# Kernel tuning notes

Hardware: AMD Instinct MI355X
Metric: run time of the kernel (lower is better)

Reference implementation:

```python
import jax, jax.numpy as jnp
import numpy as np

N_NODES = 50000
N_EDGES = 800000
D = 128
N_STEPS = 3
N_ETYPES = 4


def setup_inputs() -> dict:
    key = jax.random.key(0)
    ks = jax.random.split(key, 8)
    feat = jax.random.normal(ks[0], (N_NODES, D), dtype=jnp.float32)
    # per-edge-type linear weights, xavier-ish scale
    W_lin = jax.random.normal(ks[1], (N_ETYPES, D, D), dtype=jnp.float32) * (1.0 / np.sqrt(D))
    b_lin = jnp.zeros((N_ETYPES, D), dtype=jnp.float32)
    # GRUCell params (torch layout: [3*D, D] rows ordered r, z, n)
    s = 1.0 / np.sqrt(D)
    w_ih = jax.random.uniform(ks[2], (3 * D, D), dtype=jnp.float32, minval=-s, maxval=s)
    w_hh = jax.random.uniform(ks[3], (3 * D, D), dtype=jnp.float32, minval=-s, maxval=s)
    b_ih = jax.random.uniform(ks[4], (3 * D,), dtype=jnp.float32, minval=-s, maxval=s)
    b_hh = jax.random.uniform(ks[5], (3 * D,), dtype=jnp.float32, minval=-s, maxval=s)
    src = jax.random.randint(ks[6], (N_EDGES,), 0, N_NODES, dtype=jnp.int32)
    dst = jax.random.randint(ks[7], (N_EDGES,), 0, N_NODES, dtype=jnp.int32)
    etypes = jax.random.randint(jax.random.fold_in(key, 99), (N_EDGES,), 0, N_ETYPES, dtype=jnp.int32)
    return {"feat": feat, "W_lin": W_lin, "b_lin": b_lin, "w_ih": w_ih,
            "w_hh": w_hh, "b_ih": b_ih, "b_hh": b_hh,
            "src": src, "dst": dst, "etypes": etypes}


def _gru_cell(a, h, w_ih, w_hh, b_ih, b_hh):
    # torch.nn.GRUCell math; gates ordered r, z, n
    gi = a @ w_ih.T + b_ih   # [N, 3D]
    gh = h @ w_hh.T + b_hh   # [N, 3D]
    ir, iz, inn = jnp.split(gi, 3, axis=-1)
    hr, hz, hn = jnp.split(gh, 3, axis=-1)
    r = jax.nn.sigmoid(ir + hr)
    z = jax.nn.sigmoid(iz + hz)
    n = jnp.tanh(inn + r * hn)
    return (1.0 - z) * n + z * h


def reference(feat, W_lin, b_lin, w_ih, w_hh, b_ih, b_hh, src, dst, etypes):
    n_nodes = feat.shape[0]
    h = feat  # in_feats == out_feats, so zero_pad is empty
    for _ in range(N_STEPS):
        hs = h[src]  # gather source node features [E, D]
        # per-edge-type linear: W_etype @ h_src + b_etype
        m = jnp.zeros_like(hs)
        for i in range(N_ETYPES):
            mi = hs @ W_lin[i].T + b_lin[i]
            m = jnp.where((etypes == i)[:, None], mi, m)
        # sparse sum aggregation onto destination nodes
        a = jax.ops.segment_sum(m, dst, num_segments=n_nodes)
        h = _gru_cell(a, h, w_ih, w_hh, b_ih, b_hh)
    return h
```

## Files before the change

kernel.cpp:

```cpp
#include <hip/hip_runtime.h>
#include <hip/hip_bf16.h>
#include <math.h>
#include <stdint.h>

#define NNODES 50000
#define NEDGES 800000
#define DIM 128
#define NB_SCAN 98

typedef __attribute__((ext_vector_type(8))) short bf16x8;
typedef __attribute__((ext_vector_type(4))) float f32x4;

__device__ __forceinline__ short f2bf(float f) {
    unsigned int u = __float_as_uint(f);
    u += 0x7FFFu + ((u >> 16) & 1u);
    return (short)(u >> 16);
}

__global__ __launch_bounds__(256)
void conv_swz_w(const float* __restrict__ W, unsigned short* __restrict__ out,
                int nunits) {
    const int u = blockIdx.x * 256 + threadIdx.x;
    if (u >= nunits) return;
    const int cb = u >> 11;
    const int ul = u & 2047;
    const int fi = ul >> 8;
    const int ks = (ul >> 6) & 3;
    const int ln = ul & 63;
    const int row = cb * 128 + fi * 16 + (ln & 15);
    const int col = ks * 32 + (ln >> 4) * 8;
    const float4 f0 = *(const float4*)(W + (size_t)row * DIM + col);
    const float4 f1 = *(const float4*)(W + (size_t)row * DIM + col + 4);
    bf16x8 v;
    v[0] = f2bf(f0.x); v[1] = f2bf(f0.y); v[2] = f2bf(f0.z); v[3] = f2bf(f0.w);
    v[4] = f2bf(f1.x); v[5] = f2bf(f1.y); v[6] = f2bf(f1.z); v[7] = f2bf(f1.w);
    *(bf16x8*)(out + (size_t)u * 8) = v;
}

template<typename InT, typename OutT>
__global__ __launch_bounds__(256, 2)
void gemm_mfma_bias(const InT* __restrict__ A, const unsigned short* __restrict__ Bswz,
                    const float* __restrict__ bias, OutT* __restrict__ C,
                    int M, int N) {
    __shared__ short lsA[128 * 128];
    __shared__ short lsB[128 * 128];
    const int t = threadIdx.x;
    const int bm = blockIdx.x * 128;
    const int bn = blockIdx.y * 128;

    const unsigned short* Bblk = Bswz + (size_t)blockIdx.y * (2048 * 8);
    #pragma unroll
    for (int i = 0; i < 8; ++i) {
        const int u = i * 256 + t;
        *(bf16x8*)(lsB + (size_t)u * 8) = *(const bf16x8*)(Bblk + (size_t)u * 8);
    }
    #pragma unroll
    for (int i = 0; i < 8; ++i) {
        const int u = i * 256 + t;
        const int fi = u >> 8;
        const int ks = (u >> 6) & 3;
        const int ln = u & 63;
        const int r = ln & 15;
        const int gk = ks * 32 + (ln >> 4) * 8;
        const int grow = bm + fi * 16 + r;
        bf16x8 va = {0, 0, 0, 0, 0, 0, 0, 0};
        if (grow < M) {
            if constexpr (sizeof(InT) == 2) {
                va = *(const bf16x8*)(A + (size_t)grow * DIM + gk);
            } else {
                const float4 f0 = *(const float4*)(A + (size_t)grow * DIM + gk);
                const float4 f1 = *(const float4*)(A + (size_t)grow * DIM + gk + 4);
                va[0] = f2bf(f0.x); va[1] = f2bf(f0.y); va[2] = f2bf(f0.z); va[3] = f2bf(f0.w);
                va[4] = f2bf(f1.x); va[5] = f2bf(f1.y); va[6] = f2bf(f1.z); va[7] = f2bf(f1.w);
            }
        }
        *(bf16x8*)(lsA + (size_t)u * 8) = va;
    }
    __syncthreads();

    const int lane = t & 63;
    const int wave = t >> 6;
    const int wm = wave >> 1;
    const int wn = wave & 1;

    f32x4 acc[4][4];
    #pragma unroll
    for (int mi = 0; mi < 4; ++mi)
        #pragma unroll
        for (int nj = 0; nj < 4; ++nj)
            acc[mi][nj] = (f32x4){0.f, 0.f, 0.f, 0.f};

    #pragma unroll
    for (int ks = 0; ks < 4; ++ks) {
        bf16x8 af[4], bfr[4];
        #pragma unroll
        for (int mi = 0; mi < 4; ++mi)
            af[mi] = *(const bf16x8*)(lsA + (size_t)((((wm * 4 + mi) * 4 + ks) * 64 + lane)) * 8);
        #pragma unroll
        for (int nj = 0; nj < 4; ++nj)
            bfr[nj] = *(const bf16x8*)(lsB + (size_t)((((wn * 4 + nj) * 4 + ks) * 64 + lane)) * 8);
        #pragma unroll
        for (int mi = 0; mi < 4; ++mi)
            #pragma unroll
            for (int nj = 0; nj < 4; ++nj)
                acc[mi][nj] = __builtin_amdgcn_mfma_f32_16x16x32_bf16(
                    af[mi], bfr[nj], acc[mi][nj], 0, 0, 0);
    }

    const int cr = lane >> 4;
    const int cc = lane & 15;
    float bv[4];
    #pragma unroll
    for (int nj = 0; nj < 4; ++nj)
        bv[nj] = bias[bn + wn * 64 + nj * 16 + cc];

    #pragma unroll
    for (int mi = 0; mi < 4; ++mi) {
        const int row0 = bm + wm * 64 + mi * 16 + cr * 4;
        #pragma unroll
        for (int reg = 0; reg < 4; ++reg) {
            const int row = row0 + reg;
            if (row >= M) continue;
            #pragma unroll
            for (int nj = 0; nj < 4; ++nj) {
                const int col = bn + wn * 64 + nj * 16 + cc;
                const float v = acc[mi][nj][reg] + bv[nj];
                if constexpr (sizeof(OutT) == 2)
                    C[(size_t)row * N + col] = (OutT)f2bf(v);
                else
                    C[(size_t)row * N + col] = v;
            }
        }
    }
}

__global__ __launch_bounds__(256)
void hist_dst(const int* __restrict__ dst, int* __restrict__ cnt) {
    const int e = blockIdx.x * 256 + threadIdx.x;
    if (e < NEDGES) atomicAdd(&cnt[dst[e]], 1);
}

__global__ __launch_bounds__(256)
void scan_blksum(const int* __restrict__ cnt, int* __restrict__ partial) {
    __shared__ int red[256];
    const int b = blockIdx.x, t = threadIdx.x;
    const int i0 = b * 512 + t * 2;
    const int v0 = (i0 < NNODES) ? cnt[i0] : 0;
    const int v1 = (i0 + 1 < NNODES) ? cnt[i0 + 1] : 0;
    red[t] = v0 + v1;
    __syncthreads();
    for (int off = 128; off > 0; off >>= 1) {
        if (t < off) red[t] += red[t + off];
        __syncthreads();
    }
    if (t == 0) partial[b] = red[0];
}

__global__ __launch_bounds__(128)
void scan_partials(const int* __restrict__ partial, int* __restrict__ bloff) {
    __shared__ int s[128];
    const int t = threadIdx.x;
    s[t] = (t < NB_SCAN) ? partial[t] : 0;
    __syncthreads();
    for (int off = 1; off < 128; off <<= 1) {
        const int v = (t >= off) ? s[t - off] : 0;
        __syncthreads();
        s[t] += v;
        __syncthreads();
    }
    if (t < NB_SCAN) bloff[t] = (t == 0) ? 0 : s[t - 1];
}

__global__ __launch_bounds__(256)
void scan_final(const int* __restrict__ cnt, const int* __restrict__ bloff,
                int* __restrict__ row_start, int* __restrict__ cursor) {
    __shared__ int s[256];
    const int b = blockIdx.x, t = threadIdx.x;
    const int i0 = b * 512 + t * 2;
    const int v0 = (i0 < NNODES) ? cnt[i0] : 0;
    const int v1 = (i0 + 1 < NNODES) ? cnt[i0 + 1] : 0;
    s[t] = v0 + v1;
    __syncthreads();
    for (int off = 1; off < 256; off <<= 1) {
        const int v = (t >= off) ? s[t - off] : 0;
        __syncthreads();
        s[t] += v;
        __syncthreads();
    }
    const int excl = bloff[b] + ((t == 0) ? 0 : s[t - 1]);
    if (i0 < NNODES) { row_start[i0] = excl; cursor[i0] = excl; }
    if (i0 + 1 < NNODES) { row_start[i0 + 1] = excl + v0; cursor[i0 + 1] = excl + v0; }
    if (b == 0 && t == 0) row_start[NNODES] = NEDGES;
}

__global__ __launch_bounds__(256)
void scatter_edges(const int* __restrict__ src, const int* __restrict__ dst,
                   const int* __restrict__ et, int* __restrict__ cursor,
                   int* __restrict__ perm) {
    const int e = blockIdx.x * 256 + threadIdx.x;
    if (e >= NEDGES) return;
    const int d = dst[e];
    const int pos = atomicAdd(&cursor[d], 1);
    perm[pos] = src[e] | (et[e] << 16);
}

__global__ __launch_bounds__(256)
void edge_agg(const unsigned short* __restrict__ Ybf, const int* __restrict__ perm,
              const int* __restrict__ row_start, unsigned short* __restrict__ abf) {
    const int node = blockIdx.x * 4 + (threadIdx.x >> 6);
    const int lane = threadIdx.x & 63;
    if (node >= NNODES) return;
    const int beg = row_start[node];
    const int end = row_start[node + 1];
    float ax = 0.f, ay = 0.f;
    const int l2 = lane * 2;
    int i = beg;
    for (; i + 8 <= end; i += 8) {
        const int p0 = perm[i + 0], p1 = perm[i + 1], p2 = perm[i + 2], p3 = perm[i + 3];
        const int p4 = perm[i + 4], p5 = perm[i + 5], p6 = perm[i + 6], p7 = perm[i + 7];
        const unsigned int u0 = *(const unsigned int*)(Ybf + (size_t)(p0 & 0xFFFF) * 512 + (p0 >> 16) * DIM + l2);
        const unsigned int u1 = *(const unsigned int*)(Ybf + (size_t)(p1 & 0xFFFF) * 512 + (p1 >> 16) * DIM + l2);
        const unsigned int u2 = *(const unsigned int*)(Ybf + (size_t)(p2 & 0xFFFF) * 512 + (p2 >> 16) * DIM + l2);
        const unsigned int u3 = *(const unsigned int*)(Ybf + (size_t)(p3 & 0xFFFF) * 512 + (p3 >> 16) * DIM + l2);
        const unsigned int u4 = *(const unsigned int*)(Ybf + (size_t)(p4 & 0xFFFF) * 512 + (p4 >> 16) * DIM + l2);
        const unsigned int u5 = *(const unsigned int*)(Ybf + (size_t)(p5 & 0xFFFF) * 512 + (p5 >> 16) * DIM + l2);
        const unsigned int u6 = *(const unsigned int*)(Ybf + (size_t)(p6 & 0xFFFF) * 512 + (p6 >> 16) * DIM + l2);
        const unsigned int u7 = *(const unsigned int*)(Ybf + (size_t)(p7 & 0xFFFF) * 512 + (p7 >> 16) * DIM + l2);
        ax += __uint_as_float(u0 << 16); ay += __uint_as_float(u0 & 0xFFFF0000u);
        ax += __uint_as_float(u1 << 16); ay += __uint_as_float(u1 & 0xFFFF0000u);
        ax += __uint_as_float(u2 << 16); ay += __uint_as_float(u2 & 0xFFFF0000u);
        ax += __uint_as_float(u3 << 16); ay += __uint_as_float(u3 & 0xFFFF0000u);
        ax += __uint_as_float(u4 << 16); ay += __uint_as_float(u4 & 0xFFFF0000u);
        ax += __uint_as_float(u5 << 16); ay += __uint_as_float(u5 & 0xFFFF0000u);
        ax += __uint_as_float(u6 << 16); ay += __uint_as_float(u6 & 0xFFFF0000u);
        ax += __uint_as_float(u7 << 16); ay += __uint_as_float(u7 & 0xFFFF0000u);
    }
    for (; i < end; ++i) {
        const int p = perm[i];
        const unsigned int u = *(const unsigned int*)(Ybf + (size_t)(p & 0xFFFF) * 512 + (p >> 16) * DIM + l2);
        ax += __uint_as_float(u << 16);
        ay += __uint_as_float(u & 0xFFFF0000u);
    }
    const unsigned int bx = (unsigned short)f2bf(ax);
    const unsigned int by = (unsigned short)f2bf(ay);
    *(unsigned int*)(abf + (size_t)node * DIM + l2) = (by << 16) | bx;
}

__device__ __forceinline__ float sigf(float x) { return 1.f / (1.f + expf(-x)); }

__global__ __launch_bounds__(256)
void gru_gate(const float* __restrict__ gi, const float* __restrict__ gh,
              const float* __restrict__ h_in, float* __restrict__ h_out) {
    const int idx = blockIdx.x * 256 + threadIdx.x;
    const int v = idx >> 5;
    const int q = (idx & 31) << 2;
    if (v >= NNODES) return;
    const size_t gbase = (size_t)v * 384 + q;
    const float4 ir = *(const float4*)(gi + gbase);
    const float4 iz = *(const float4*)(gi + gbase + 128);
    const float4 in4 = *(const float4*)(gi + gbase + 256);
    const float4 hr = *(const float4*)(gh + gbase);
    const float4 hz = *(const float4*)(gh + gbase + 128);
    const float4 hn = *(const float4*)(gh + gbase + 256);
    const float4 h4 = *(const float4*)(h_in + (size_t)v * DIM + q);
    float4 o;
    {
        const float r = sigf(ir.x + hr.x);
        const float z = sigf(iz.x + hz.x);
        const float n = tanhf(in4.x + r * hn.x);
        o.x = (1.f - z) * n + z * h4.x;
    }
    {
        const float r = sigf(ir.y + hr.y);
        const float z = sigf(iz.y + hz.y);
        const float n = tanhf(in4.y + r * hn.y);
        o.y = (1.f - z) * n + z * h4.y;
    }
    {
        const float r = sigf(ir.z + hr.z);
        const float z = sigf(iz.z + hz.z);
        const float n = tanhf(in4.z + r * hn.z);
        o.z = (1.f - z) * n + z * h4.z;
    }
    {
        const float r = sigf(ir.w + hr.w);
        const float z = sigf(iz.w + hz.w);
        const float n = tanhf(in4.w + r * hn.w);
        o.w = (1.f - z) * n + z * h4.w;
    }
    *(float4*)(h_out + (size_t)v * DIM + q) = o;
}

extern "C" void kernel_launch(void* const* d_in, const int* in_sizes, int n_in,
                              void* d_out, int out_size, void* d_ws, size_t ws_size,
                              hipStream_t stream) {
    const float* feat  = (const float*)d_in[0];
    const float* W_lin = (const float*)d_in[1];
    const float* b_lin = (const float*)d_in[2];
    const float* w_ih  = (const float*)d_in[3];
    const float* w_hh  = (const float*)d_in[4];
    const float* b_ih  = (const float*)d_in[5];
    const float* b_hh  = (const float*)d_in[6];
    const int*   src   = (const int*)d_in[7];
    const int*   dst   = (const int*)d_in[8];
    const int*   et    = (const int*)d_in[9];
    float* out = (float*)d_out;

    float* h  = (float*)d_ws;
    float* Yf = h + (size_t)NNODES * DIM;
    unsigned short* Y = (unsigned short*)Yf;
    float* abase = Yf + (size_t)NNODES * 512;
    unsigned short* abf = (unsigned short*)abase;
    float* gi = Yf;
    float* gh = gi + (size_t)NNODES * 384;
    int* row_start = (int*)(gh + (size_t)NNODES * 384);
    int* perm      = row_start + (NNODES + 1);
    int* partial   = perm + NEDGES;
    int* bloff     = partial + NB_SCAN;
    unsigned short* wswz = (unsigned short*)(((uintptr_t)(bloff + NB_SCAN) + 15) & ~(uintptr_t)15);
    unsigned short* wlin_swz = wswz;
    unsigned short* wih_swz  = wswz + 65536;
    unsigned short* whh_swz  = wih_swz + 49152;
    int* cnt    = (int*)abase;
    int* cursor = cnt + NNODES + 64;

    const dim3 blk(256);
    const int mblocks = (NNODES + 127) / 128;
    const int eblocks = (NEDGES + 255) / 256;

    conv_swz_w<<<dim3(32), blk, 0, stream>>>(W_lin, wlin_swz, 8192);
    conv_swz_w<<<dim3(24), blk, 0, stream>>>(w_ih, wih_swz, 6144);
    conv_swz_w<<<dim3(24), blk, 0, stream>>>(w_hh, whh_swz, 6144);
    hipMemsetAsync(cnt, 0, (size_t)NNODES * sizeof(int), stream);
    hist_dst<<<dim3(eblocks), blk, 0, stream>>>(dst, cnt);
    scan_blksum<<<dim3(NB_SCAN), blk, 0, stream>>>(cnt, partial);
    scan_partials<<<dim3(1), dim3(128), 0, stream>>>(partial, bloff);
    scan_final<<<dim3(NB_SCAN), blk, 0, stream>>>(cnt, bloff, row_start, cursor);
    scatter_edges<<<dim3(eblocks), blk, 0, stream>>>(src, dst, et, cursor, perm);

    for (int s = 0; s < 3; ++s) {
        const float* h_in = (s == 0) ? feat : h;
        float* h_out = (s == 2) ? out : h;

        gemm_mfma_bias<float, unsigned short><<<dim3(mblocks, 4), blk, 0, stream>>>(
            h_in, wlin_swz, b_lin, Y, NNODES, 512);
        edge_agg<<<dim3((NNODES + 3) / 4), blk, 0, stream>>>(Y, perm, row_start, abf);
        gemm_mfma_bias<unsigned short, float><<<dim3(mblocks, 3), blk, 0, stream>>>(
            abf, wih_swz, b_ih, gi, NNODES, 384);
        gemm_mfma_bias<float, float><<<dim3(mblocks, 3), blk, 0, stream>>>(
            h_in, whh_swz, b_hh, gh, NNODES, 384);
        gru_gate<<<dim3((NNODES * 32 + 255) / 256), blk, 0, stream>>>(gi, gh, h_in, h_out);
    }
}
```

Baseline: 673.3 us.

## Fuse GRU input and hidden GEMMs into one K=256 GEMM over concatenated bf16 [a|h]

Stores the aggregated messages and the hidden state side by side as one bf16 buffer [a|h] and multiplies it once by a combined 256x512 weight. In that weight the r and z gates sum the w_ih and w_hh parts, and the n gate keeps its input and hidden halves separate. This removes one GEMM launch, lets the r/z pre-activations be added inside the accumulator, and cuts the gate kernel's reads from six gate vectors to four. The GRU gate kernel now also writes a bf16 copy of h, so the next step's GEMMs read bf16 instead of fp32. The cost is a K-loop with two LDS load phases and extra syncs, plus zero-padded MFMA work for the n-gate blocks.

```diff
diff --git a/kernel.cpp b/kernel.cpp
--- a/kernel.cpp
+++ b/kernel.cpp
@@ -37,47 +37,72 @@
     *(bf16x8*)(out + (size_t)u * 8) = v;
 }
 
-template<typename InT, typename OutT>
+__global__ __launch_bounds__(256)
+void conv_swz_wbig(const float* __restrict__ w_ih, const float* __restrict__ w_hh,
+                   unsigned short* __restrict__ out) {
+    const int u = blockIdx.x * 256 + threadIdx.x;
+    if (u >= 16384) return;
+    const int nb = u >> 12;
+    const int kb = (u >> 11) & 1;
+    const int ul = u & 2047;
+    const int fi = ul >> 8;
+    const int ks = (ul >> 6) & 3;
+    const int ln = ul & 63;
+    const int nrow = nb * 128 + fi * 16 + (ln & 15);
+    const int kc0 = ks * 32 + (ln >> 4) * 8;
+    bf16x8 v;
+    #pragma unroll
+    for (int j = 0; j < 8; ++j) {
+        const int kc = kb * 128 + kc0 + j;
+        float f = 0.f;
+        if (nrow < 256) {
+            f = (kc < 128) ? w_ih[(size_t)nrow * DIM + kc]
+                           : w_hh[(size_t)nrow * DIM + (kc - 128)];
+        } else if (nrow < 384) {
+            if (kc < 128) f = w_ih[(size_t)nrow * DIM + kc];
+        } else {
+            if (kc >= 128) f = w_hh[(size_t)(nrow - 128) * DIM + (kc - 128)];
+        }
+        v[j] = f2bf(f);
+    }
+    *(bf16x8*)(out + (size_t)u * 8) = v;
+}
+
+__global__ __launch_bounds__(256)
+void build_bias_big(const float* __restrict__ b_ih, const float* __restrict__ b_hh,
+                    float* __restrict__ bias_big) {
+    const int n = blockIdx.x * 256 + threadIdx.x;
+    if (n >= 512) return;
+    float b;
+    if (n < 256)      b = b_ih[n] + b_hh[n];
+    else if (n < 384) b = b_ih[n];
+    else              b = b_hh[n - 128];
+    bias_big[n] = b;
+}
+
+__global__ __launch_bounds__(256)
+void feat2bf(const float* __restrict__ feat, unsigned short* __restrict__ ah) {
+    const int idx = blockIdx.x * 256 + threadIdx.x;
+    const int v = idx >> 5;
+    const int q = (idx & 31) << 2;
+    if (v >= NNODES) return;
+    const float4 f = *(const float4*)(feat + (size_t)v * DIM + q);
+    ushort4 o;
+    o.x = (unsigned short)f2bf(f.x); o.y = (unsigned short)f2bf(f.y);
+    o.z = (unsigned short)f2bf(f.z); o.w = (unsigned short)f2bf(f.w);
+    *(ushort4*)(ah + (size_t)v * 256 + 128 + q) = o;
+}
+
+template<int KB, typename OutT>
 __global__ __launch_bounds__(256, 2)
-void gemm_mfma_bias(const InT* __restrict__ A, const unsigned short* __restrict__ Bswz,
+void gemm_mfma_bias(const unsigned short* __restrict__ A, int lda,
+                    const unsigned short* __restrict__ Bswz,
                     const float* __restrict__ bias, OutT* __restrict__ C,
                     int M, int N) {
     __shared__ short lsA[128 * 128];
     __shared__ short lsB[128 * 128];
     const int t = threadIdx.x;
     const int bm = blockIdx.x * 128;
-    const int bn = blockIdx.y * 128;
-
-    const unsigned short* Bblk = Bswz + (size_t)blockIdx.y * (2048 * 8);
-    #pragma unroll
-    for (int i = 0; i < 8; ++i) {
-        const int u = i * 256 + t;
-        *(bf16x8*)(lsB + (size_t)u * 8) = *(const bf16x8*)(Bblk + (size_t)u * 8);
-    }
-    #pragma unroll
-    for (int i = 0; i < 8; ++i) {
-        const int u = i * 256 + t;
-        const int fi = u >> 8;
-        const int ks = (u >> 6) & 3;
-        const int ln = u & 63;
-        const int r = ln & 15;
-        const int gk = ks * 32 + (ln >> 4) * 8;
-        const int grow = bm + fi * 16 + r;
-        bf16x8 va = {0, 0, 0, 0, 0, 0, 0, 0};
-        if (grow < M) {
-            if constexpr (sizeof(InT) == 2) {
-                va = *(const bf16x8*)(A + (size_t)grow * DIM + gk);
-            } else {
-                const float4 f0 = *(const float4*)(A + (size_t)grow * DIM + gk);
-                const float4 f1 = *(const float4*)(A + (size_t)grow * DIM + gk + 4);
-                va[0] = f2bf(f0.x); va[1] = f2bf(f0.y); va[2] = f2bf(f0.z); va[3] = f2bf(f0.w);
-                va[4] = f2bf(f1.x); va[5] = f2bf(f1.y); va[6] = f2bf(f1.z); va[7] = f2bf(f1.w);
-            }
-        }
-        *(bf16x8*)(lsA + (size_t)u * 8) = va;
-    }
-    __syncthreads();
-
     const int lane = t & 63;
     const int wave = t >> 6;
     const int wm = wave >> 1;
@@ -90,23 +115,48 @@
         for (int nj = 0; nj < 4; ++nj)
             acc[mi][nj] = (f32x4){0.f, 0.f, 0.f, 0.f};
 
-    #pragma unroll
-    for (int ks = 0; ks < 4; ++ks) {
-        bf16x8 af[4], bfr[4];
-        #pragma unroll
-        for (int mi = 0; mi < 4; ++mi)
-            af[mi] = *(const bf16x8*)(lsA + (size_t)((((wm * 4 + mi) * 4 + ks) * 64 + lane)) * 8);
-        #pragma unroll
-        for (int nj = 0; nj < 4; ++nj)
-            bfr[nj] = *(const bf16x8*)(lsB + (size_t)((((wn * 4 + nj) * 4 + ks) * 64 + lane)) * 8);
-        #pragma unroll
-        for (int mi = 0; mi < 4; ++mi)
+    for (int kb = 0; kb < KB; ++kb) {
+        if (kb) __syncthreads();
+        const unsigned short* Bblk = Bswz + ((size_t)blockIdx.y * KB + kb) * (2048 * 8);
+        #pragma unroll
+        for (int i = 0; i < 8; ++i) {
+            const int u = i * 256 + t;
+            *(bf16x8*)(lsB + (size_t)u * 8) = *(const bf16x8*)(Bblk + (size_t)u * 8);
+        }
+        #pragma unroll
+        for (int i = 0; i < 8; ++i) {
+            const int u = i * 256 + t;
+            const int fi = u >> 8;
+            const int ks = (u >> 6) & 3;
+            const int ln = u & 63;
+            const int r = ln & 15;
+            const int gk = kb * 128 + ks * 32 + (ln >> 4) * 8;
+            const int grow = bm + fi * 16 + r;
+            bf16x8 va = {0, 0, 0, 0, 0, 0, 0, 0};
+            if (grow < M) va = *(const bf16x8*)(A + (size_t)grow * lda + gk);
+            *(bf16x8*)(lsA + (size_t)u * 8) = va;
+        }
+        __syncthreads();
+
+        #pragma unroll
+        for (int ks = 0; ks < 4; ++ks) {
+            bf16x8 af[4], bfr[4];
+            #pragma unroll
+            for (int mi = 0; mi < 4; ++mi)
+                af[mi] = *(const bf16x8*)(lsA + (size_t)((((wm * 4 + mi) * 4 + ks) * 64 + lane)) * 8);
             #pragma unroll
             for (int nj = 0; nj < 4; ++nj)
-                acc[mi][nj] = __builtin_amdgcn_mfma_f32_16x16x32_bf16(
-                    af[mi], bfr[nj], acc[mi][nj], 0, 0, 0);
-    }
-
+                bfr[nj] = *(const bf16x8*)(lsB + (size_t)((((wn * 4 + nj) * 4 + ks) * 64 + lane)) * 8);
+            #pragma unroll
+            for (int mi = 0; mi < 4; ++mi)
+                #pragma unroll
+                for (int nj = 0; nj < 4; ++nj)
+                    acc[mi][nj] = __builtin_amdgcn_mfma_f32_16x16x32_bf16(
+                        af[mi], bfr[nj], acc[mi][nj], 0, 0, 0);
+        }
+    }
+
+    const int bn = blockIdx.y * 128;
     const int cr = lane >> 4;
     const int cc = lane & 15;
     float bv[4];
@@ -206,7 +256,7 @@
 
 __global__ __launch_bounds__(256)
 void edge_agg(const unsigned short* __restrict__ Ybf, const int* __restrict__ perm,
-              const int* __restrict__ row_start, unsigned short* __restrict__ abf) {
+              const int* __restrict__ row_start, unsigned short* __restrict__ ah) {
     const int node = blockIdx.x * 4 + (threadIdx.x >> 6);
     const int lane = threadIdx.x & 63;
     if (node >= NNODES) return;
@@ -243,52 +293,50 @@
     }
     const unsigned int bx = (unsigned short)f2bf(ax);
     const unsigned int by = (unsigned short)f2bf(ay);
-    *(unsigned int*)(abf + (size_t)node * DIM + l2) = (by << 16) | bx;
+    *(unsigned int*)(ah + (size_t)node * 256 + l2) = (by << 16) | bx;
 }
 
 __device__ __forceinline__ float sigf(float x) { return 1.f / (1.f + expf(-x)); }
 
 __global__ __launch_bounds__(256)
-void gru_gate(const float* __restrict__ gi, const float* __restrict__ gh,
-              const float* __restrict__ h_in, float* __restrict__ h_out) {
+void gru_gate(const float* __restrict__ g, const float* __restrict__ h_in,
+              float* __restrict__ h_out, unsigned short* __restrict__ ah) {
     const int idx = blockIdx.x * 256 + threadIdx.x;
     const int v = idx >> 5;
     const int q = (idx & 31) << 2;
     if (v >= NNODES) return;
-    const size_t gbase = (size_t)v * 384 + q;
-    const float4 ir = *(const float4*)(gi + gbase);
-    const float4 iz = *(const float4*)(gi + gbase + 128);
-    const float4 in4 = *(const float4*)(gi + gbase + 256);
-    const float4 hr = *(const float4*)(gh + gbase);
-    const float4 hz = *(const float4*)(gh + gbase + 128);
-    const float4 hn = *(const float4*)(gh + gbase + 256);
+    const size_t gb = (size_t)v * 512 + q;
+    const float4 rs = *(const float4*)(g + gb);
+    const float4 zs = *(const float4*)(g + gb + 128);
+    const float4 in4 = *(const float4*)(g + gb + 256);
+    const float4 hn = *(const float4*)(g + gb + 384);
     const float4 h4 = *(const float4*)(h_in + (size_t)v * DIM + q);
     float4 o;
     {
-        const float r = sigf(ir.x + hr.x);
-        const float z = sigf(iz.x + hz.x);
+        const float r = sigf(rs.x), z = sigf(zs.x);
         const float n = tanhf(in4.x + r * hn.x);
         o.x = (1.f - z) * n + z * h4.x;
     }
     {
-        const float r = sigf(ir.y + hr.y);
-        const float z = sigf(iz.y + hz.y);
+        const float r = sigf(rs.y), z = sigf(zs.y);
         const float n = tanhf(in4.y + r * hn.y);
         o.y = (1.f - z) * n + z * h4.y;
     }
     {
-        const float r = sigf(ir.z + hr.z);
-        const float z = sigf(iz.z + hz.z);
+        const float r = sigf(rs.z), z = sigf(zs.z);
         const float n = tanhf(in4.z + r * hn.z);
         o.z = (1.f - z) * n + z * h4.z;
     }
     {
-        const float r = sigf(ir.w + hr.w);
-        const float z = sigf(iz.w + hz.w);
+        const float r = sigf(rs.w), z = sigf(zs.w);
         const float n = tanhf(in4.w + r * hn.w);
         o.w = (1.f - z) * n + z * h4.w;
     }
     *(float4*)(h_out + (size_t)v * DIM + q) = o;
+    ushort4 ob;
+    ob.x = (unsigned short)f2bf(o.x); ob.y = (unsigned short)f2bf(o.y);
+    ob.z = (unsigned short)f2bf(o.z); ob.w = (unsigned short)f2bf(o.w);
+    *(ushort4*)(ah + (size_t)v * 256 + 128 + q) = ob;
 }
 
 extern "C" void kernel_launch(void* const* d_in, const int* in_sizes, int n_in,
@@ -307,21 +355,18 @@
     float* out = (float*)d_out;
 
     float* h  = (float*)d_ws;
-    float* Yf = h + (size_t)NNODES * DIM;
-    unsigned short* Y = (unsigned short*)Yf;
-    float* abase = Yf + (size_t)NNODES * 512;
-    unsigned short* abf = (unsigned short*)abase;
-    float* gi = Yf;
-    float* gh = gi + (size_t)NNODES * 384;
-    int* row_start = (int*)(gh + (size_t)NNODES * 384);
+    float* Yg = h + (size_t)NNODES * DIM;
+    unsigned short* Y = (unsigned short*)Yg;
+    float* g  = Yg;
+    unsigned short* ah = (unsigned short*)(Yg + (size_t)NNODES * 512);
+    int* row_start = (int*)((float*)ah + (size_t)NNODES * 128);
     int* perm      = row_start + (NNODES + 1);
     int* partial   = perm + NEDGES;
     int* bloff     = partial + NB_SCAN;
-    unsigned short* wswz = (unsigned short*)(((uintptr_t)(bloff + NB_SCAN) + 15) & ~(uintptr_t)15);
-    unsigned short* wlin_swz = wswz;
-    unsigned short* wih_swz  = wswz + 65536;
-    unsigned short* whh_swz  = wih_swz + 49152;
-    int* cnt    = (int*)abase;
+    unsigned short* wlin_swz = (unsigned short*)(((uintptr_t)(bloff + NB_SCAN) + 15) & ~(uintptr_t)15);
+    unsigned short* wbig_swz = wlin_swz + 65536;
+    float* bias_big = (float*)(wbig_swz + 131072);
+    int* cnt    = (int*)Yg;
     int* cursor = cnt + NNODES + 64;
 
     const dim3 blk(256);
@@ -329,8 +374,9 @@
     const int eblocks = (NEDGES + 255) / 256;
 
     conv_swz_w<<<dim3(32), blk, 0, stream>>>(W_lin, wlin_swz, 8192);
-    conv_swz_w<<<dim3(24), blk, 0, stream>>>(w_ih, wih_swz, 6144);
-    conv_swz_w<<<dim3(24), blk, 0, stream>>>(w_hh, whh_swz, 6144);
+    conv_swz_wbig<<<dim3(64), blk, 0, stream>>>(w_ih, w_hh, wbig_swz);
+    build_bias_big<<<dim3(2), blk, 0, stream>>>(b_ih, b_hh, bias_big);
+    feat2bf<<<dim3((NNODES * 32 + 255) / 256), blk, 0, stream>>>(feat, ah);
     hipMemsetAsync(cnt, 0, (size_t)NNODES * sizeof(int), stream);
     hist_dst<<<dim3(eblocks), blk, 0, stream>>>(dst, cnt);
     scan_blksum<<<dim3(NB_SCAN), blk, 0, stream>>>(cnt, partial);
@@ -342,13 +388,11 @@
         const float* h_in = (s == 0) ? feat : h;
         float* h_out = (s == 2) ? out : h;
 
-        gemm_mfma_bias<float, unsigned short><<<dim3(mblocks, 4), blk, 0, stream>>>(
-            h_in, wlin_swz, b_lin, Y, NNODES, 512);
-        edge_agg<<<dim3((NNODES + 3) / 4), blk, 0, stream>>>(Y, perm, row_start, abf);
-        gemm_mfma_bias<unsigned short, float><<<dim3(mblocks, 3), blk, 0, stream>>>(
-            abf, wih_swz, b_ih, gi, NNODES, 384);
-        gemm_mfma_bias<float, float><<<dim3(mblocks, 3), blk, 0, stream>>>(
-            h_in, whh_swz, b_hh, gh, NNODES, 384);
-        gru_gate<<<dim3((NNODES * 32 + 255) / 256), blk, 0, stream>>>(gi, gh, h_in, h_out);
-    }
-}
+        gemm_mfma_bias<1, unsigned short><<<dim3(mblocks, 4), blk, 0, stream>>>(
+            ah + 128, 256, wlin_swz, b_lin, Y, NNODES, 512);
+        edge_agg<<<dim3((NNODES + 3) / 4), blk, 0, stream>>>(Y, perm, row_start, ah);
+        gemm_mfma_bias<2, float><<<dim3(mblocks, 4), blk, 0, stream>>>(
+            ah, 256, wbig_swz, bias_big, g, NNODES, 512);
+        gru_gate<<<dim3((NNODES * 32 + 255) / 256), blk, 0, stream>>>(g, h_in, h_out, ah);
+    }
+}
```

New measurement: 621.2 us. -7.7%, faster.
